# Kernel tuning notes

Measured on AMD Instinct MI355X. Metric: run time of the kernel, lower is better.

Reference implementation:

```python
import jax, jax.numpy as jnp
import numpy as np


def setup_inputs() -> dict:
    key = jax.random.key(0)
    ks = jax.random.split(key, 8)
    N, E = 10000, 160000
    IN, OUT, TC = 512, 512, 256
    x = jax.random.normal(ks[0], (N, IN), dtype=jnp.float32)
    t_emb = jax.random.normal(ks[1], (TC,), dtype=jnp.float32)
    edge_index = jax.random.randint(ks[2], (2, E), 0, N, dtype=jnp.int64)
    # GCNConv weight (glorot-ish scale) and bias
    W = jax.random.normal(ks[3], (IN, OUT), dtype=jnp.float32) / np.sqrt(IN)
    b = jnp.zeros((OUT,), dtype=jnp.float32)
    # time_proj Linear(TC, OUT)
    Wt = jax.random.normal(ks[4], (TC, OUT), dtype=jnp.float32) / np.sqrt(TC)
    bt = jnp.zeros((OUT,), dtype=jnp.float32)
    return {"x": x, "t_emb": t_emb, "edge_index": edge_index,
            "W": W, "b": b, "Wt": Wt, "bt": bt}


def _gcn_conv(x, edge_index, W, b):
    # PyG GCNConv: add self-loops, symmetric normalization, xW, scatter-add, +bias
    N = x.shape[0]
    loops = jnp.arange(N, dtype=edge_index.dtype)
    src = jnp.concatenate([edge_index[0], loops])  # [E+N]
    dst = jnp.concatenate([edge_index[1], loops])
    deg = jax.ops.segment_sum(jnp.ones_like(dst, dtype=x.dtype), dst,
                              num_segments=N)  # in-degree incl. self-loop
    dinv = jnp.where(deg > 0, jax.lax.rsqrt(deg), 0.0)
    norm = dinv[src] * dinv[dst]  # [E+N]
    xw = x @ W  # [N, OUT] - transform before gather (fewer FLOPs on edges)
    msgs = norm[:, None] * xw[src]  # [E+N, OUT]
    out = jax.ops.segment_sum(msgs, dst, num_segments=N)
    return out + b


def reference(x, t_emb, edge_index, W, b, Wt, bt):
    h = _gcn_conv(x, edge_index, W, b)          # [N, OUT]
    time_emb = t_emb @ Wt + bt                   # [OUT] (1-D t_emb branch)
    return h + time_emb
```

## Files before the change

### kernel.cpp

```cpp
#include <hip/hip_runtime.h>

#define OUTC 512
#define INC 512
#define NTILE 4
#define TCOL 128
#define TPB 256
#define CAP 96

typedef __bf16 bf16x8 __attribute__((ext_vector_type(8)));
typedef float f32x4 __attribute__((ext_vector_type(4)));

typedef __attribute__((address_space(1))) const unsigned char as1_u8;
typedef __attribute__((address_space(3))) unsigned char as3_u8;
static __device__ __forceinline__ void gload16(const void* g, void* l) {
    __builtin_amdgcn_global_load_lds((as1_u8*)g, (as3_u8*)l, 16, 0, 0);
}

static __device__ __forceinline__ unsigned short f2bf(float f) {
    unsigned u = __float_as_uint(f);
    unsigned r = u + 0x7fffu + ((u >> 16) & 1u);
    return (unsigned short)(r >> 16);
}
static __device__ __forceinline__ float bflo(unsigned r) { return __uint_as_float(r << 16); }
static __device__ __forceinline__ float bfhi(unsigned r) { return __uint_as_float(r & 0xffff0000u); }
static __device__ __forceinline__ void acc8s(float* a, uint4 v, float n) {
    a[0] += n * bflo(v.x); a[1] += n * bfhi(v.x);
    a[2] += n * bflo(v.y); a[3] += n * bfhi(v.y);
    a[4] += n * bflo(v.z); a[5] += n * bfhi(v.z);
    a[6] += n * bflo(v.w); a[7] += n * bfhi(v.w);
}

__global__ __launch_bounds__(256) void k_prep(const float* __restrict__ x,
                                              const float* __restrict__ W,
                                              const float* __restrict__ t_emb,
                                              const float* __restrict__ Wt,
                                              const float* __restrict__ bt,
                                              const float* __restrict__ b,
                                              int* __restrict__ counts,
                                              unsigned short* __restrict__ xb,
                                              unsigned short* __restrict__ wtb,
                                              float* __restrict__ temb,
                                              int ZB, int XBB,
                                              int M, int Mpad, int TC) {
    __shared__ float smem[32 * 33];
    int bid = blockIdx.x;
    if (bid < ZB) {
        int i = bid * 256 + threadIdx.x;
        if (i < M) counts[i] = 0;
    } else if (bid < ZB + XBB) {
        int idx = (bid - ZB) * 256 + threadIdx.x;
        int row = idx >> 6;
        int kg = (idx & 63) * 8;
        ushort4 h0 = make_ushort4(0, 0, 0, 0), h1 = make_ushort4(0, 0, 0, 0);
        if (row < M) {
            float4 v0 = *(const float4*)(x + (size_t)row * INC + kg);
            float4 v1 = *(const float4*)(x + (size_t)row * INC + kg + 4);
            h0 = make_ushort4(f2bf(v0.x), f2bf(v0.y), f2bf(v0.z), f2bf(v0.w));
            h1 = make_ushort4(f2bf(v1.x), f2bf(v1.y), f2bf(v1.z), f2bf(v1.w));
        }
        *(ushort4*)(xb + (size_t)row * INC + kg) = h0;
        *(ushort4*)(xb + (size_t)row * INC + kg + 4) = h1;
    } else if (bid < ZB + XBB + 256) {
        int b2 = bid - (ZB + XBB);
        int bk = (b2 & 15) * 32, bn = (b2 >> 4) * 32;
        int tx = threadIdx.x & 31, ty = threadIdx.x >> 5;
        for (int r = ty; r < 32; r += 8)
            smem[r * 33 + tx] = W[(size_t)(bk + r) * OUTC + bn + tx];
        __syncthreads();
        for (int r = ty; r < 32; r += 8)
            wtb[(size_t)(bn + r) * INC + bk + tx] = f2bf(smem[tx * 33 + r]);
    } else {
        int j = bid - (ZB + XBB + 256);
        int t = threadIdx.x;
        float p = 0.0f;
        for (int k = t; k < TC; k += 256) p += t_emb[k] * Wt[(size_t)k * OUTC + j];
        smem[t] = p;
        __syncthreads();
        for (int s = 128; s > 0; s >>= 1) {
            if (t < s) smem[t] += smem[t + s];
            __syncthreads();
        }
        if (t == 0) temb[j] = smem[0] + bt[j] + b[j];
    }
}

__global__ __launch_bounds__(256) void k_ag(const unsigned short* __restrict__ xb,
                                            const unsigned short* __restrict__ wtb,
                                            unsigned short* __restrict__ xwb,
                                            const int* __restrict__ src,
                                            const int* __restrict__ dst,
                                            int* __restrict__ counts,
                                            int* __restrict__ slots,
                                            int E, int Mpad) {
    __shared__ unsigned short lsA[2][128 * 64];
    __shared__ unsigned short lsB[2][128 * 64];

    const int bid = blockIdx.x;
    const int tid = threadIdx.x;
    const int GB = (Mpad / 128) * (OUTC / 128);

    if (bid >= GB) {
        int e = (bid - GB) * 256 + tid;
        if (e < E) {
            int s = src[e];
            int d = dst[e];
            int pos = atomicAdd(&counts[d], 1);
            if (pos < CAP) slots[(size_t)d * CAP + pos] = s;
        }
        return;
    }

    const int n0 = (bid & 3) * 128;
    const int m0 = (bid >> 2) * 128;
    const int lane = tid & 63;
    const int wave = tid >> 6;
    const int wr = (wave >> 1) * 64;
    const int wc = (wave & 1) * 64;
    const int l15 = lane & 15;
    const int qb = lane >> 4;

    const int l8r = lane >> 3;
    const int swb = ((lane & 7) ^ l8r) << 4;

    const unsigned char* gA[4];
    const unsigned char* gB[4];
#pragma unroll
    for (int i = 0; i < 4; ++i) {
        int c = wave * 4 + i;
        int row = c * 8 + l8r;
        gA[i] = (const unsigned char*)(xb + (size_t)(m0 + row) * INC) + swb;
        gB[i] = (const unsigned char*)(wtb + (size_t)(n0 + row) * INC) + swb;
    }

    f32x4 acc[4][4];
#pragma unroll
    for (int m = 0; m < 4; ++m)
#pragma unroll
        for (int n = 0; n < 4; ++n)
            acc[m][n] = (f32x4){0.f, 0.f, 0.f, 0.f};

    unsigned short* pa = &lsA[0][0];
    unsigned short* pb = &lsB[0][0];
    unsigned short* qa = &lsA[1][0];
    unsigned short* qbf = &lsB[1][0];

#define STAGE(dA, dB, kb)                                                    \
    {                                                                        \
        _Pragma("unroll")                                                    \
        for (int i = 0; i < 4; ++i) {                                        \
            int c = wave * 4 + i;                                            \
            gload16(gA[i] + (kb) * 2, (unsigned char*)(dA) + c * 1024);      \
            gload16(gB[i] + (kb) * 2, (unsigned char*)(dB) + c * 1024);      \
        }                                                                    \
    }

    STAGE(pa, pb, 0);
    __syncthreads();

    for (int t = 0; t < INC / 64; ++t) {
        if (t < INC / 64 - 1) STAGE(qa, qbf, (t + 1) * 64);

#pragma unroll
        for (int kc = 0; kc < 64; kc += 32) {
            const int q = (kc >> 3) + qb;
            bf16x8 af[4], bv[4];
#pragma unroll
            for (int m = 0; m < 4; ++m) {
                int row = wr + m * 16 + l15;
                af[m] = *(const bf16x8*)((const unsigned char*)pa + row * 128 +
                                         ((q ^ (row & 7)) << 4));
            }
#pragma unroll
            for (int n = 0; n < 4; ++n) {
                int row = wc + n * 16 + l15;
                bv[n] = *(const bf16x8*)((const unsigned char*)pb + row * 128 +
                                         ((q ^ (row & 7)) << 4));
            }
#pragma unroll
            for (int m = 0; m < 4; ++m)
#pragma unroll
                for (int n = 0; n < 4; ++n)
                    acc[m][n] = __builtin_amdgcn_mfma_f32_16x16x32_bf16(af[m], bv[n], acc[m][n], 0, 0, 0);
        }

        __syncthreads();
        unsigned short* tmp;
        tmp = pa; pa = qa; qa = tmp;
        tmp = pb; pb = qbf; qbf = tmp;
    }
#undef STAGE

    const int rbase = (lane >> 4) * 4;
#pragma unroll
    for (int m = 0; m < 4; ++m)
#pragma unroll
        for (int n = 0; n < 4; ++n) {
            int gcol = n0 + wc + n * 16 + l15;
            unsigned short* p = xwb + (size_t)(gcol >> 7) * Mpad * TCOL + (gcol & 127);
#pragma unroll
            for (int r = 0; r < 4; ++r) {
                int grow = m0 + wr + m * 16 + rbase + r;
                p[(size_t)grow * TCOL] = f2bf(acc[m][n][r]);
            }
        }
}

__global__ __launch_bounds__(256) void k_gather(const int* __restrict__ slots,
                                                const int* __restrict__ counts,
                                                const unsigned short* __restrict__ xwb,
                                                const float* __restrict__ temb,
                                                float* __restrict__ out, int N, int Mpad) {
    const int bid = blockIdx.x;
    const int tile = (bid & 7) >> 1;
    const int node = (bid >> 3) * 8 + (bid & 1) * 4 + (threadIdx.x >> 6);
    if (node >= N) return;
    const int lane = threadIdx.x & 63;
    const int slot = lane >> 4;
    const int c8 = (lane & 15) * 8;
    const unsigned short* basep = xwb + (size_t)tile * Mpad * TCOL + c8;

    float a[8] = {0.f, 0.f, 0.f, 0.f, 0.f, 0.f, 0.f, 0.f};
    const int deg = counts[node];
    const int dc = deg < CAP ? deg : CAP;
    const int* sp = slots + (size_t)node * CAP;
    int i = 0;
    for (; i + 8 <= dc; i += 8) {
        int sA = sp[i + slot];
        int sB = sp[i + 4 + slot];
        uint4 vA = *(const uint4*)(basep + (size_t)sA * TCOL);
        uint4 vB = *(const uint4*)(basep + (size_t)sB * TCOL);
        float nA = rsqrtf((float)counts[sA] + 1.0f);
        float nB = rsqrtf((float)counts[sB] + 1.0f);
        acc8s(a, vA, nA);
        acc8s(a, vB, nB);
    }
    for (; i < dc; i += 4) {
        int idx = i + slot;
        int sA = node;
        float nA = 0.f;
        if (idx < dc) {
            sA = sp[idx];
            nA = rsqrtf((float)counts[sA] + 1.0f);
        }
        uint4 v = *(const uint4*)(basep + (size_t)sA * TCOL);
        acc8s(a, v, nA);
    }
#pragma unroll
    for (int k = 0; k < 8; ++k) {
        a[k] += __shfl_xor(a[k], 16, 64);
        a[k] += __shfl_xor(a[k], 32, 64);
    }
    const float di = rsqrtf((float)deg + 1.0f);
    {
        uint4 v = *(const uint4*)(basep + (size_t)node * TCOL);
        acc8s(a, v, di);
    }
    if (slot < 2) {
        const int gc = tile * TCOL + c8 + slot * 4;
        float4 tv = *(const float4*)(temb + gc);
        float4 o;
        o.x = di * a[slot * 4 + 0] + tv.x;
        o.y = di * a[slot * 4 + 1] + tv.y;
        o.z = di * a[slot * 4 + 2] + tv.z;
        o.w = di * a[slot * 4 + 3] + tv.w;
        *(float4*)(out + (size_t)node * OUTC + gc) = o;
    }
}

extern "C" void kernel_launch(void* const* d_in, const int* in_sizes, int n_in,
                              void* d_out, int out_size, void* d_ws, size_t ws_size,
                              hipStream_t stream) {
    const float* x     = (const float*)d_in[0];
    const float* t_emb = (const float*)d_in[1];
    const int*   ei    = (const int*)d_in[2];
    const float* W     = (const float*)d_in[3];
    const float* b     = (const float*)d_in[4];
    const float* Wt    = (const float*)d_in[5];
    const float* bt    = (const float*)d_in[6];
    float* out = (float*)d_out;

    const int N  = in_sizes[0] / INC;
    const int E  = in_sizes[2] / 2;
    const int TC = in_sizes[1];
    const int Mpad = (N + 127) & ~127;

    char* ws = (char*)d_ws;
    size_t off = 0;
    unsigned short* xb  = (unsigned short*)(ws + off); off += (size_t)Mpad * INC * 2;
    unsigned short* xwb = (unsigned short*)(ws + off); off += (size_t)Mpad * OUTC * 2;
    unsigned short* wtb = (unsigned short*)(ws + off); off += (size_t)INC * OUTC * 2;
    int* counts = (int*)(ws + off);        off += ((size_t)N * 4 + 255) & ~(size_t)255;
    int* slots  = (int*)(ws + off);        off += ((size_t)N * CAP * 4 + 255) & ~(size_t)255;
    float* temb = (float*)(ws + off);      off += OUTC * 4;

    const int* srcIdx = ei;
    const int* dstIdx = ei + E;

    const int ZB  = (N + 255) / 256;
    const int XBB = Mpad * (INC / 8) / 256;
    const int GB  = (Mpad / 128) * (OUTC / 128);
    const int SB  = (E + 255) / 256;

    k_prep<<<ZB + XBB + 256 + OUTC, TPB, 0, stream>>>(x, W, t_emb, Wt, bt, b,
                                                      counts, xb, wtb, temb,
                                                      ZB, XBB, N, Mpad, TC);
    k_ag<<<GB + SB, TPB, 0, stream>>>(xb, wtb, xwb, srcIdx, dstIdx,
                                      counts, slots, E, Mpad);

    const int gather_blocks = ((N + 7) / 8) * 8;
    k_gather<<<gather_blocks, TPB, 0, stream>>>(slots, counts, xwb,
                                                temb, out, N, Mpad);
}
```

Before: 127.0 us.

## Store XW row-major and gather one node per block with LDS reduction

The bf16 XW buffer now uses a plain row-major [node, 512] layout instead of four column tiles of 128. The gather kernel assigns one node per 256-thread block. Each of the four waves reads whole 1 KB neighbour rows, strided across edges, and the per-wave partial sums are combined through shared memory. The aim is longer contiguous gathers and no cross-tile redundancy in index and degree loads, at the cost of an LDS reduction with a __syncthreads per node and less work per block.

```diff
diff --git a/kernel.cpp b/kernel.cpp
--- a/kernel.cpp
+++ b/kernel.cpp
@@ -2,8 +2,6 @@
 
 #define OUTC 512
 #define INC 512
-#define NTILE 4
-#define TCOL 128
 #define TPB 256
 #define CAP 96
 
@@ -196,11 +194,10 @@
 #pragma unroll
         for (int n = 0; n < 4; ++n) {
             int gcol = n0 + wc + n * 16 + l15;
-            unsigned short* p = xwb + (size_t)(gcol >> 7) * Mpad * TCOL + (gcol & 127);
 #pragma unroll
             for (int r = 0; r < 4; ++r) {
                 int grow = m0 + wr + m * 16 + rbase + r;
-                p[(size_t)grow * TCOL] = f2bf(acc[m][n][r]);
+                xwb[(size_t)grow * OUTC + gcol] = f2bf(acc[m][n][r]);
             }
         }
 }
@@ -209,62 +206,55 @@
                                                 const int* __restrict__ counts,
                                                 const unsigned short* __restrict__ xwb,
                                                 const float* __restrict__ temb,
-                                                float* __restrict__ out, int N, int Mpad) {
-    const int bid = blockIdx.x;
-    const int tile = (bid & 7) >> 1;
-    const int node = (bid >> 3) * 8 + (bid & 1) * 4 + (threadIdx.x >> 6);
-    if (node >= N) return;
-    const int lane = threadIdx.x & 63;
-    const int slot = lane >> 4;
-    const int c8 = (lane & 15) * 8;
-    const unsigned short* basep = xwb + (size_t)tile * Mpad * TCOL + c8;
-
-    float a[8] = {0.f, 0.f, 0.f, 0.f, 0.f, 0.f, 0.f, 0.f};
+                                                float* __restrict__ out, int N) {
+    __shared__ float red[4 * 512];
+    const int node = blockIdx.x;
+    const int tid = threadIdx.x;
+    const int lane = tid & 63;
+    const int wave = tid >> 6;
+
     const int deg = counts[node];
     const int dc = deg < CAP ? deg : CAP;
     const int* sp = slots + (size_t)node * CAP;
-    int i = 0;
-    for (; i + 8 <= dc; i += 8) {
-        int sA = sp[i + slot];
-        int sB = sp[i + 4 + slot];
-        uint4 vA = *(const uint4*)(basep + (size_t)sA * TCOL);
-        uint4 vB = *(const uint4*)(basep + (size_t)sB * TCOL);
-        float nA = rsqrtf((float)counts[sA] + 1.0f);
-        float nB = rsqrtf((float)counts[sB] + 1.0f);
-        acc8s(a, vA, nA);
-        acc8s(a, vB, nB);
-    }
-    for (; i < dc; i += 4) {
-        int idx = i + slot;
-        int sA = node;
-        float nA = 0.f;
-        if (idx < dc) {
-            sA = sp[idx];
-            nA = rsqrtf((float)counts[sA] + 1.0f);
-        }
-        uint4 v = *(const uint4*)(basep + (size_t)sA * TCOL);
-        acc8s(a, v, nA);
-    }
-#pragma unroll
-    for (int k = 0; k < 8; ++k) {
-        a[k] += __shfl_xor(a[k], 16, 64);
-        a[k] += __shfl_xor(a[k], 32, 64);
-    }
+
+    float a[8] = {0.f, 0.f, 0.f, 0.f, 0.f, 0.f, 0.f, 0.f};
+    int i = wave;
+    for (; i + 4 < dc; i += 8) {
+        int s0 = sp[i];
+        int s1 = sp[i + 4];
+        uint4 v0 = *(const uint4*)(xwb + (size_t)s0 * OUTC + lane * 8);
+        uint4 v1 = *(const uint4*)(xwb + (size_t)s1 * OUTC + lane * 8);
+        float n0 = rsqrtf((float)counts[s0] + 1.0f);
+        float n1 = rsqrtf((float)counts[s1] + 1.0f);
+        acc8s(a, v0, n0);
+        acc8s(a, v1, n1);
+    }
+    if (i < dc) {
+        int s0 = sp[i];
+        uint4 v0 = *(const uint4*)(xwb + (size_t)s0 * OUTC + lane * 8);
+        acc8s(a, v0, rsqrtf((float)counts[s0] + 1.0f));
+    }
+
+    float* rw = red + wave * 512;
+#pragma unroll
+    for (int k = 0; k < 8; ++k) rw[k * 64 + lane] = a[k];
+    __syncthreads();
+
     const float di = rsqrtf((float)deg + 1.0f);
-    {
-        uint4 v = *(const uint4*)(basep + (size_t)node * TCOL);
-        acc8s(a, v, di);
-    }
-    if (slot < 2) {
-        const int gc = tile * TCOL + c8 + slot * 4;
-        float4 tv = *(const float4*)(temb + gc);
-        float4 o;
-        o.x = di * a[slot * 4 + 0] + tv.x;
-        o.y = di * a[slot * 4 + 1] + tv.y;
-        o.z = di * a[slot * 4 + 2] + tv.z;
-        o.w = di * a[slot * 4 + 3] + tv.w;
-        *(float4*)(out + (size_t)node * OUTC + gc) = o;
-    }
+    const int c0 = tid * 2;
+    const int c1 = c0 + 1;
+    unsigned selfw = *(const unsigned*)(xwb + (size_t)node * OUTC + c0);
+    float2 tv = *(const float2*)(temb + c0);
+    float e0 = 0.f, e1 = 0.f;
+#pragma unroll
+    for (int w = 0; w < 4; ++w) {
+        e0 += red[w * 512 + (c0 & 7) * 64 + (c0 >> 3)];
+        e1 += red[w * 512 + (c1 & 7) * 64 + (c1 >> 3)];
+    }
+    float2 o;
+    o.x = di * (e0 + di * bflo(selfw)) + tv.x;
+    o.y = di * (e1 + di * bfhi(selfw)) + tv.y;
+    *(float2*)(out + (size_t)node * OUTC + c0) = o;
 }
 
 extern "C" void kernel_launch(void* const* d_in, const int* in_sizes, int n_in,
@@ -307,7 +297,5 @@
     k_ag<<<GB + SB, TPB, 0, stream>>>(xb, wtb, xwb, srcIdx, dstIdx,
                                       counts, slots, E, Mpad);
 
-    const int gather_blocks = ((N + 7) / 8) * 8;
-    k_gather<<<gather_blocks, TPB, 0, stream>>>(slots, counts, xwb,
-                                                temb, out, N, Mpad);
-}
+    k_gather<<<N, TPB, 0, stream>>>(slots, counts, xwb, temb, out, N);
+}
```

Result: faster. 123.7 us (median of 2 runs) (-2.5%).
